# Optimization experiments

Measured on AMD Instinct MI355X. Metric: run time of the kernel, lower is better.

The kernel has to match this reference:

```python
import jax, jax.numpy as jnp
import numpy as np


def _fwht_last(x):
    """Unnormalized fast Walsh-Hadamard transform (natural/Hadamard order)
    along the last axis via log2(n) butterfly stages. n must be a power of 2."""
    n = x.shape[-1]
    lead = x.shape[:-1]
    x = x.reshape((-1, n))
    h = 1
    while h < n:  # fixed log2(n) iterations, unrolled under jit
        x = x.reshape((-1, n // (2 * h), 2, h))
        a, b = x[:, :, 0, :], x[:, :, 1, :]
        x = jnp.stack([a + b, a - b], axis=2).reshape((-1, n))
        h *= 2
    return x.reshape(lead + (n,))


def _fwht_axis(x, axis):
    x = jnp.moveaxis(x, axis, -1)
    x = _fwht_last(x)
    return jnp.moveaxis(x, -1, axis)


def setup_inputs() -> dict:
    key = jax.random.key(0)
    # [B, H, W, C] channels-last, as read in WHT2CUDAFunction.forward
    x = jax.random.normal(key, (64, 64, 64, 128), dtype=jnp.float32)
    return {"x": x}


def reference(x):
    # Dual-output 2D Walsh-Hadamard butterfly transform:
    # transIm1 = WHT applied along H (row transform, intermediate)
    # transIm2 = WHT of transIm1 along W (full separable 2D WHT)
    trans_im1 = _fwht_axis(x, 1)
    trans_im2 = _fwht_axis(trans_im1, 2)
    return (trans_im1, trans_im2)
```

## Files before the change

kernel.cpp:

```cpp
#include <hip/hip_runtime.h>


template <int TSTRIDE, int FSTRIDE>
__global__ __launch_bounds__(256) void fwht64_kernel(const float* __restrict__ in,
                                                     float* __restrict__ out) {
    const int tid = blockIdx.x * 256 + threadIdx.x;
    const int c   = tid & 127;
    const int m   = (tid >> 7) & 63;
    const int b0  = tid >> 13;
    const int base = b0 * (64 * 64 * 128) + m * FSTRIDE + c;

    float v[64];
#pragma unroll
    for (int k = 0; k < 64; ++k)
        v[k] = in[base + k * TSTRIDE];

#pragma unroll
    for (int sh = 0; sh < 6; ++sh) {
        const int h = 1 << sh;
#pragma unroll
        for (int s = 0; s < 64; s += 2 * h) {
#pragma unroll
            for (int t = 0; t < h; ++t) {
                const float a = v[s + t];
                const float b = v[s + t + h];
                v[s + t]     = a + b;
                v[s + t + h] = a - b;
            }
        }
    }

#pragma unroll
    for (int k = 0; k < 64; ++k)
        out[base + k * TSTRIDE] = v[k];
}

extern "C" void kernel_launch(void* const* d_in, const int* in_sizes, int n_in,
                              void* d_out, int out_size, void* d_ws, size_t ws_size,
                              hipStream_t stream) {
    const float* x = (const float*)d_in[0];
    float* out0 = (float*)d_out;
    float* out1 = out0 + 64 * 64 * 64 * 128;

    const int blocks = 2048;

    fwht64_kernel<8192, 128><<<blocks, 256, 0, stream>>>(x, out0);
    fwht64_kernel<128, 8192><<<blocks, 256, 0, stream>>>(out0, out1);
}
```

Before: 366.6 us.

## Stage FWHT lines through LDS tiles with vectorized float4 global access

Each block loads a 64x256 tile into shared memory with float4 global loads, performs the 64-point Walsh-Hadamard butterflies per thread from LDS, writes back to LDS, then stores with float4. This aims to widen global memory transactions and improve streaming efficiency versus scalar strided accesses. It adds two LDS round trips and a large shared-memory footprint that limits occupancy.

```diff
diff --git a/kernel.cpp b/kernel.cpp
--- a/kernel.cpp
+++ b/kernel.cpp
@@ -1,19 +1,31 @@
 #include <hip/hip_runtime.h>
 
 
-template <int TSTRIDE, int FSTRIDE>
-__global__ __launch_bounds__(256) void fwht64_kernel(const float* __restrict__ in,
-                                                     float* __restrict__ out) {
-    const int tid = blockIdx.x * 256 + threadIdx.x;
-    const int c   = tid & 127;
-    const int m   = (tid >> 7) & 63;
-    const int b0  = tid >> 13;
-    const int base = b0 * (64 * 64 * 128) + m * FSTRIDE + c;
+#define PITCH 260
+
+template <int TSTRIDE, int FOUT, int PAIR_MUL>
+__global__ __launch_bounds__(256) void fwht64_lds(const float* __restrict__ in,
+                                                  float* __restrict__ out) {
+    __shared__ float tile[64 * PITCH];
+    const int t    = threadIdx.x;
+    const int b0   = blockIdx.x >> 5;
+    const int pair = blockIdx.x & 31;
+    const int base = b0 * 524288 + pair * PAIR_MUL;
+
+#pragma unroll
+    for (int k = 0; k < 16; ++k) {
+        const int idx = k * 256 + t;
+        const int row = idx >> 6;
+        const int f   = (idx & 63) * 4;
+        const int fo  = (f >> 7) * FOUT + (f & 127);
+        const float4 v = *(const float4*)(in + base + row * TSTRIDE + fo);
+        *(float4*)(&tile[row * PITCH + f]) = v;
+    }
+    __syncthreads();
 
     float v[64];
 #pragma unroll
-    for (int k = 0; k < 64; ++k)
-        v[k] = in[base + k * TSTRIDE];
+    for (int r = 0; r < 64; ++r) v[r] = tile[r * PITCH + t];
 
 #pragma unroll
     for (int sh = 0; sh < 6; ++sh) {
@@ -21,18 +33,28 @@
 #pragma unroll
         for (int s = 0; s < 64; s += 2 * h) {
 #pragma unroll
-            for (int t = 0; t < h; ++t) {
-                const float a = v[s + t];
-                const float b = v[s + t + h];
-                v[s + t]     = a + b;
-                v[s + t + h] = a - b;
+            for (int u = 0; u < h; ++u) {
+                const float a = v[s + u];
+                const float b = v[s + u + h];
+                v[s + u]     = a + b;
+                v[s + u + h] = a - b;
             }
         }
     }
 
 #pragma unroll
-    for (int k = 0; k < 64; ++k)
-        out[base + k * TSTRIDE] = v[k];
+    for (int r = 0; r < 64; ++r) tile[r * PITCH + t] = v[r];
+    __syncthreads();
+
+#pragma unroll
+    for (int k = 0; k < 16; ++k) {
+        const int idx = k * 256 + t;
+        const int row = idx >> 6;
+        const int f   = (idx & 63) * 4;
+        const int fo  = (f >> 7) * FOUT + (f & 127);
+        *(float4*)(out + base + row * TSTRIDE + fo) =
+            *(const float4*)(&tile[row * PITCH + f]);
+    }
 }
 
 extern "C" void kernel_launch(void* const* d_in, const int* in_sizes, int n_in,
@@ -42,8 +64,9 @@
     float* out0 = (float*)d_out;
     float* out1 = out0 + 64 * 64 * 64 * 128;
 
-    const int blocks = 2048;
+    const int blocks = 64 * 32;
 
-    fwht64_kernel<8192, 128><<<blocks, 256, 0, stream>>>(x, out0);
-    fwht64_kernel<128, 8192><<<blocks, 256, 0, stream>>>(out0, out1);
+    fwht64_lds<8192, 128, 256><<<blocks, 256, 0, stream>>>(x, out0);
+
+    fwht64_lds<128, 8192, 16384><<<blocks, 256, 0, stream>>>(out0, out1);
 }
```

Measured after the change: 367.1 us. About the same (+0.1%).
